# Optimization experiments

Measured on AMD Instinct MI355X. Metric: run time of the kernel, lower is better.

Reference implementation:

```python
import jax, jax.numpy as jnp
import numpy as np

DIM = 768; HEADS = 12; HD = DIM // HEADS; SCALE = HD ** -0.5
B = 4; T = 8; H = 14; W = 14; N = H * W  # 196 VMAE patches per frame
DOWN = 192   # adapter down dim = dim * 0.25
MLP_H = 3072 # dim * mlp_ratio

def _ln(x, g, b, eps=1e-5):
    m = x.mean(-1, keepdims=True)
    v = ((x - m) ** 2).mean(-1, keepdims=True)
    return (x - m) * jax.lax.rsqrt(v + eps) * g + b

def _lin(x, w, b=None):
    y = x @ w.T
    return y if b is None else y + b

def _gelu(x):
    return jax.nn.gelu(x, approximate=False)  # torch nn.GELU (erf)

def _mha(q, k, v):  # q:[b,h,n,d] k,v:[b,h,m,d]
    a = jax.nn.softmax((q * SCALE) @ jnp.swapaxes(k, -2, -1), axis=-1)
    return a @ v

def _adapter(x, w1, b1, w2, b2, skip):
    y = _lin(_gelu(_lin(x, w1, b1)), w2, b2)
    return x + y if skip else y

def _block(s_x, t_x, p):
    # --- self-attention on temporal (VMAE) tokens, with adapter ---
    xn = _ln(t_x, p['g1'], p['bb1'])
    bias = jnp.concatenate([p['q_bias'], jnp.zeros_like(p['v_bias']), p['v_bias']])
    Bx, Nx, _ = xn.shape
    qkv = _lin(xn, p['qkv_w'], bias).reshape(Bx, Nx, 3, HEADS, HD).transpose(2, 0, 3, 1, 4)
    o = _mha(qkv[0], qkv[1], qkv[2]).transpose(0, 2, 1, 3).reshape(Bx, Nx, DIM)
    o = _lin(o, p['aproj_w'], p['aproj_b'])
    t = t_x + _adapter(o, p['sa_w1'], p['sa_b1'], p['sa_w2'], p['sa_b2'], True)
    # --- S2T cross-attn: temporal queries attend to per-frame CNN spatial tokens ---
    s_pat = s_x.reshape(B * T, H * W, DIM) + p['s2t_pos_cnn']
    tx = t.reshape(B * T, N, DIM) + p['s2t_pos_vmae']
    q = _lin(tx, p['s2t_qw'], p['s2t_qb']).reshape(B * T, N, HEADS, HD).transpose(0, 2, 1, 3)
    kv = _lin(s_pat, p['s2t_kvw'], p['s2t_kvb']).reshape(B * T, H * W, 2, HEADS, HD).transpose(2, 0, 3, 1, 4)
    o = _mha(q, kv[0], kv[1]).transpose(0, 2, 1, 3).reshape(B * T, N, DIM)
    o = _lin(o, p['s2t_pw'], p['s2t_pb']).reshape(B, T * N, DIM)
    t = t + o
    # --- T2S cross-attn: per-location CNN queries attend over time to VMAE tokens ---
    s_pat = s_x.reshape(B, T, H * W, DIM).transpose(0, 2, 1, 3) + p['t2s_pos_cnn']  # b hw t c
    tx = t.reshape(B, T, N, DIM).transpose(0, 2, 1, 3) + p['t2s_pos_vmae']          # b n t d (N==H*W)
    s_pat = s_pat.reshape(B * H * W, T, DIM)
    tx = tx.reshape(B * N, T, DIM)
    q = _lin(s_pat, p['t2s_qw'], p['t2s_qb']).reshape(B * H * W, T, HEADS, HD).transpose(0, 2, 1, 3)
    kv = _lin(tx, p['t2s_kvw'], p['t2s_kvb']).reshape(B * N, T, 2, HEADS, HD).transpose(2, 0, 3, 1, 4)
    o = _mha(q, kv[0], kv[1]).transpose(0, 2, 1, 3).reshape(B * H * W, T, DIM)
    o = _lin(o, p['t2s_pw'], p['t2s_pb'])
    s = s_x + o.reshape(B, H, W, T, DIM).transpose(0, 3, 1, 2, 4).reshape(B * T, H, W, DIM)
    # --- MLP + parallel adapter (scale = 0.5 per Block.__init__) ---
    xn2 = _ln(t, p['g2'], p['bb2'])
    t = t + _lin(_gelu(_lin(xn2, p['fc1_w'], p['fc1_b'])), p['fc2_w'], p['fc2_b']) \
          + 0.5 * _adapter(xn2, p['ma_w1'], p['ma_b1'], p['ma_w2'], p['ma_b2'], False)
    return s, t

PARAM_NAMES = ['g1','bb1','qkv_w','q_bias','v_bias','aproj_w','aproj_b',
               'sa_w1','sa_b1','sa_w2','sa_b2',
               's2t_pos_cnn','s2t_pos_vmae','s2t_qw','s2t_qb','s2t_kvw','s2t_kvb','s2t_pw','s2t_pb',
               't2s_pos_cnn','t2s_pos_vmae','t2s_qw','t2s_qb','t2s_kvw','t2s_kvb','t2s_pw','t2s_pb',
               'g2','bb2','fc1_w','fc1_b','fc2_w','fc2_b','ma_w1','ma_b1','ma_w2','ma_b2']

def setup_inputs():
    key = jax.random.key(0)
    ks = iter(jax.random.split(key, 64))
    def w(shape, s=0.02):
        return jax.random.normal(next(ks), shape, jnp.float32) * s
    d = dict(
        s_x=jax.random.normal(next(ks), (B * T, H, W, DIM), jnp.float32),
        t_x=jax.random.normal(next(ks), (B, T * N, DIM), jnp.float32),
        g1=jnp.ones((DIM,), jnp.float32), bb1=jnp.zeros((DIM,), jnp.float32),
        qkv_w=w((3 * DIM, DIM)), q_bias=jnp.zeros((DIM,), jnp.float32), v_bias=jnp.zeros((DIM,), jnp.float32),
        aproj_w=w((DIM, DIM)), aproj_b=jnp.zeros((DIM,), jnp.float32),
        sa_w1=w((DOWN, DIM)), sa_b1=jnp.zeros((DOWN,), jnp.float32),
        sa_w2=w((DIM, DOWN)), sa_b2=jnp.zeros((DIM,), jnp.float32),
        s2t_pos_cnn=w((H * W, DIM), SCALE), s2t_pos_vmae=w((196, DIM), SCALE),
        s2t_qw=w((DIM, DIM)), s2t_qb=jnp.zeros((DIM,), jnp.float32),
        s2t_kvw=w((2 * DIM, DIM)), s2t_kvb=jnp.zeros((2 * DIM,), jnp.float32),
        s2t_pw=w((DIM, DIM)), s2t_pb=jnp.zeros((DIM,), jnp.float32),
        t2s_pos_cnn=w((T, DIM), SCALE), t2s_pos_vmae=w((T, DIM), SCALE),
        t2s_qw=w((DIM, DIM)), t2s_qb=jnp.zeros((DIM,), jnp.float32),
        t2s_kvw=w((2 * DIM, DIM)), t2s_kvb=jnp.zeros((2 * DIM,), jnp.float32),
        t2s_pw=w((DIM, DIM)), t2s_pb=jnp.zeros((DIM,), jnp.float32),
        g2=jnp.ones((DIM,), jnp.float32), bb2=jnp.zeros((DIM,), jnp.float32),
        fc1_w=w((MLP_H, DIM)), fc1_b=jnp.zeros((MLP_H,), jnp.float32),
        fc2_w=w((DIM, MLP_H)), fc2_b=jnp.zeros((DIM,), jnp.float32),
        ma_w1=w((DOWN, DIM)), ma_b1=jnp.zeros((DOWN,), jnp.float32),
        ma_w2=w((DIM, DOWN)), ma_b2=jnp.zeros((DIM,), jnp.float32),
    )
    return d

def reference(s_x, t_x, g1, bb1, qkv_w, q_bias, v_bias, aproj_w, aproj_b,
              sa_w1, sa_b1, sa_w2, sa_b2,
              s2t_pos_cnn, s2t_pos_vmae, s2t_qw, s2t_qb, s2t_kvw, s2t_kvb, s2t_pw, s2t_pb,
              t2s_pos_cnn, t2s_pos_vmae, t2s_qw, t2s_qb, t2s_kvw, t2s_kvb, t2s_pw, t2s_pb,
              g2, bb2, fc1_w, fc1_b, fc2_w, fc2_b, ma_w1, ma_b1, ma_w2, ma_b2):
    loc = locals()
    p = {k: loc[k] for k in PARAM_NAMES}
    return _block(s_x, t_x, p)
```

## Files before the change

### kernel.cpp

```cpp
#include <hip/hip_runtime.h>
#include <hip/hip_bf16.h>
#include <math.h>


typedef __bf16 bf16_t;
typedef bf16_t bf16x4 __attribute__((ext_vector_type(4)));
typedef bf16_t bf16x8 __attribute__((ext_vector_type(8)));
typedef float  f32x4  __attribute__((ext_vector_type(4)));

typedef const __attribute__((address_space(1))) void* gas_t;
typedef __attribute__((address_space(3))) void* las_t;
__device__ __forceinline__ void async16(const void* g, void* l) {
    __builtin_amdgcn_global_load_lds((gas_t)g, (las_t)l, 16, 0, 0);
}

#define MFMA(a,b,c) __builtin_amdgcn_mfma_f32_16x16x32_bf16((a),(b),(c),0,0,0)
#define EXP2(x) __builtin_amdgcn_exp2f(x)
#define LOG2E 1.4426950408889634f

template<bool GELU>
__global__ __launch_bounds__(256) void gemm128(
    const bf16_t* __restrict__ A, const bf16_t* __restrict__ W,
    const float* __restrict__ bias,
    const float* __restrict__ res1, const float* __restrict__ res2,
    float res2_scale,
    float* __restrict__ Yf, bf16_t* __restrict__ Yb,
    int M, int N, int K)
{
    __shared__ bf16_t As[128*64];
    __shared__ bf16_t Bs[128*64];
    const int tid = threadIdx.x, wave = tid >> 6, lane = tid & 63;
    const int m0 = blockIdx.y * 128, n0 = blockIdx.x * 128;
    const int wm = (wave & 1) * 64, wn = (wave >> 1) * 64;
    const int l15 = lane & 15, lq = lane >> 4;
    const int lrow = lane >> 3, lcol = (lane & 7) * 8;

    f32x4 acc[4][4] = {};

    for (int k0 = 0; k0 < K; k0 += 64) {
#pragma unroll
        for (int c = 0; c < 4; ++c) {
            const int r = wave * 32 + c * 8;
            async16(A + (size_t)(m0 + r + lrow) * K + k0 + lcol, &As[r * 64]);
            async16(W + (size_t)(n0 + r + lrow) * K + k0 + lcol, &Bs[r * 64]);
        }
        __syncthreads();
#pragma unroll
        for (int kk = 0; kk < 64; kk += 32) {
            bf16x8 a[4], b[4];
#pragma unroll
            for (int i = 0; i < 4; ++i)
                a[i] = *(const bf16x8*)&As[(wm + i * 16 + l15) * 64 + kk + lq * 8];
#pragma unroll
            for (int i = 0; i < 4; ++i)
                b[i] = *(const bf16x8*)&Bs[(wn + i * 16 + l15) * 64 + kk + lq * 8];
#pragma unroll
            for (int mi = 0; mi < 4; ++mi)
#pragma unroll
                for (int ni = 0; ni < 4; ++ni)
                    acc[mi][ni] = MFMA(a[mi], b[ni], acc[mi][ni]);
        }
        __syncthreads();
    }

#pragma unroll
    for (int mi = 0; mi < 4; ++mi)
#pragma unroll
    for (int ni = 0; ni < 4; ++ni) {
        const int gn = n0 + wn + ni * 16 + l15;
        const float bv = bias ? bias[gn] : 0.f;
#pragma unroll
        for (int i = 0; i < 4; ++i) {
            const int gm = m0 + wm + mi * 16 + lq * 4 + i;
            float v = acc[mi][ni][i] + bv;
            if (GELU) v = 0.5f * v * (1.0f + erff(v * 0.70710678118654752f));
            const size_t off = (size_t)gm * N + gn;
            if (res1) v += res1[off];
            if (res2) v += res2_scale * res2[off];
            if (Yf) Yf[off] = v;
            if (Yb) Yb[off] = (bf16_t)v;
        }
    }
}

template<bool GELU>
__global__ __launch_bounds__(256) void gemm128x64(
    const bf16_t* __restrict__ A, const bf16_t* __restrict__ W,
    const float* __restrict__ bias,
    const float* __restrict__ res1, const float* __restrict__ res2,
    float res2_scale,
    float* __restrict__ Yf, bf16_t* __restrict__ Yb,
    int M, int N, int K)
{
    __shared__ bf16_t As[128*64];
    __shared__ bf16_t Bs[64*64];
    const int tid = threadIdx.x, wave = tid >> 6, lane = tid & 63;
    const int m0 = blockIdx.y * 128, n0 = blockIdx.x * 64;
    const int wm = (wave & 1) * 64, wn = (wave >> 1) * 32;
    const int l15 = lane & 15, lq = lane >> 4;
    const int lrow = lane >> 3, lcol = (lane & 7) * 8;

    f32x4 acc[4][2] = {};

    for (int k0 = 0; k0 < K; k0 += 64) {
#pragma unroll
        for (int c = 0; c < 4; ++c) {
            const int r = wave * 32 + c * 8;
            async16(A + (size_t)(m0 + r + lrow) * K + k0 + lcol, &As[r * 64]);
        }
#pragma unroll
        for (int c = 0; c < 2; ++c) {
            const int r = wave * 16 + c * 8;
            async16(W + (size_t)(n0 + r + lrow) * K + k0 + lcol, &Bs[r * 64]);
        }
        __syncthreads();
#pragma unroll
        for (int kk = 0; kk < 64; kk += 32) {
            bf16x8 a[4], b[2];
#pragma unroll
            for (int i = 0; i < 4; ++i)
                a[i] = *(const bf16x8*)&As[(wm + i * 16 + l15) * 64 + kk + lq * 8];
#pragma unroll
            for (int i = 0; i < 2; ++i)
                b[i] = *(const bf16x8*)&Bs[(wn + i * 16 + l15) * 64 + kk + lq * 8];
#pragma unroll
            for (int mi = 0; mi < 4; ++mi)
#pragma unroll
                for (int ni = 0; ni < 2; ++ni)
                    acc[mi][ni] = MFMA(a[mi], b[ni], acc[mi][ni]);
        }
        __syncthreads();
    }

#pragma unroll
    for (int mi = 0; mi < 4; ++mi)
#pragma unroll
    for (int ni = 0; ni < 2; ++ni) {
        const int gn = n0 + wn + ni * 16 + l15;
        const float bv = bias ? bias[gn] : 0.f;
#pragma unroll
        for (int i = 0; i < 4; ++i) {
            const int gm = m0 + wm + mi * 16 + lq * 4 + i;
            float v = acc[mi][ni][i] + bv;
            if (GELU) v = 0.5f * v * (1.0f + erff(v * 0.70710678118654752f));
            const size_t off = (size_t)gm * N + gn;
            if (res1) v += res1[off];
            if (res2) v += res2_scale * res2[off];
            if (Yf) Yf[off] = v;
            if (Yb) Yb[off] = (bf16_t)v;
        }
    }
}

template<bool GELU>
__global__ __launch_bounds__(256) void gemm_bt(
    const float* __restrict__ X, const float* __restrict__ W,
    const float* __restrict__ bias,
    const float* __restrict__ res1, const float* __restrict__ res2,
    float res2_scale,
    float* __restrict__ Y, int M, int N, int K)
{
    __shared__ bf16_t As[64][72];
    __shared__ bf16_t Bs[64][72];
    const int tid  = threadIdx.x;
    const int n0   = blockIdx.x * 64;
    const int m0   = blockIdx.y * 64;
    const int wave = tid >> 6, lane = tid & 63;
    const int wm   = (wave & 1) * 32, wn = (wave >> 1) * 32;
    const int l15  = lane & 15, lq = lane >> 4;
    f32x4 acc[2][2] = {};
    const int sr = tid >> 4;
    const int sc4 = (tid & 15) * 4;

    for (int k0 = 0; k0 < K; k0 += 64) {
#pragma unroll
        for (int i = 0; i < 4; ++i) {
            const int row = sr + i * 16;
            const float4 xv = *reinterpret_cast<const float4*>(
                X + (size_t)(m0 + row) * K + k0 + sc4);
            bf16x4 p;
            p[0] = (bf16_t)xv.x; p[1] = (bf16_t)xv.y;
            p[2] = (bf16_t)xv.z; p[3] = (bf16_t)xv.w;
            *reinterpret_cast<bf16x4*>(&As[row][sc4]) = p;
        }
#pragma unroll
        for (int i = 0; i < 4; ++i) {
            const int row = sr + i * 16;
            const float4 wv = *reinterpret_cast<const float4*>(
                W + (size_t)(n0 + row) * K + k0 + sc4);
            bf16x4 p;
            p[0] = (bf16_t)wv.x; p[1] = (bf16_t)wv.y;
            p[2] = (bf16_t)wv.z; p[3] = (bf16_t)wv.w;
            *reinterpret_cast<bf16x4*>(&Bs[row][sc4]) = p;
        }
        __syncthreads();
#pragma unroll
        for (int kk = 0; kk < 64; kk += 32) {
            bf16x8 a0 = *reinterpret_cast<const bf16x8*>(&As[wm +      l15][kk + lq * 8]);
            bf16x8 a1 = *reinterpret_cast<const bf16x8*>(&As[wm + 16 + l15][kk + lq * 8]);
            bf16x8 b0 = *reinterpret_cast<const bf16x8*>(&Bs[wn +      l15][kk + lq * 8]);
            bf16x8 b1 = *reinterpret_cast<const bf16x8*>(&Bs[wn + 16 + l15][kk + lq * 8]);
            acc[0][0] = MFMA(a0, b0, acc[0][0]);
            acc[0][1] = MFMA(a0, b1, acc[0][1]);
            acc[1][0] = MFMA(a1, b0, acc[1][0]);
            acc[1][1] = MFMA(a1, b1, acc[1][1]);
        }
        __syncthreads();
    }

#pragma unroll
    for (int mt = 0; mt < 2; ++mt)
#pragma unroll
    for (int nt = 0; nt < 2; ++nt) {
        const int gn = n0 + wn + nt * 16 + l15;
        const float bv = bias[gn];
#pragma unroll
        for (int i = 0; i < 4; ++i) {
            const int gm = m0 + wm + mt * 16 + lq * 4 + i;
            float v = acc[mt][nt][i] + bv;
            if (GELU) v = 0.5f * v * (1.0f + erff(v * 0.70710678118654752f));
            const size_t off = (size_t)gm * N + gn;
            if (res1) v += res1[off];
            if (res2) v += res2_scale * res2[off];
            Y[off] = v;
        }
    }
}

__global__ __launch_bounds__(256) void flash_k(
    const bf16_t* __restrict__ Q, int ldq,
    const bf16_t* __restrict__ Kp, int ldk,
    const bf16_t* __restrict__ Vp, int ldv,
    bf16_t* __restrict__ O, int ldo,
    int nq, int nk, float scale)
{
    __shared__ bf16_t Qs[64 * 68];
    __shared__ bf16_t Ks[64 * 68];
    __shared__ bf16_t Vs[64 * 68];

    const int tid = threadIdx.x, wave = tid >> 6, lane = tid & 63;
    const int q0 = blockIdx.x * 64, hoff = blockIdx.y * 64, g = blockIdx.z;
    const int l15 = lane & 15, lq = lane >> 4;
    const int wm16 = wave * 16;
    const int sr = tid >> 3, sc8 = (tid & 7) * 8;
    const float sl2e = scale * LOG2E;

    {
        int r0 = q0 + sr;      if (r0 > nq - 1) r0 = nq - 1;
        int r1 = q0 + sr + 32; if (r1 > nq - 1) r1 = nq - 1;
        bf16x8 a = *(const bf16x8*)(Q + ((size_t)g * nq + r0) * ldq + hoff + sc8);
        bf16x8 b = *(const bf16x8*)(Q + ((size_t)g * nq + r1) * ldq + hoff + sc8);
        *(bf16x8*)&Qs[sr * 68 + sc8] = a;
        *(bf16x8*)&Qs[(sr + 32) * 68 + sc8] = b;
    }
    float mrow[4], lrow[4];
#pragma unroll
    for (int i = 0; i < 4; ++i) { mrow[i] = -INFINITY; lrow[i] = 0.f; }
    f32x4 acc[4] = {};

    for (int kk0 = 0; kk0 < nk; kk0 += 64) {
        __syncthreads();
        {
            int r0 = kk0 + sr;      if (r0 > nk - 1) r0 = nk - 1;
            int r1 = kk0 + sr + 32; if (r1 > nk - 1) r1 = nk - 1;
            bf16x8 a = *(const bf16x8*)(Kp + ((size_t)g * nk + r0) * ldk + hoff + sc8);
            bf16x8 b = *(const bf16x8*)(Kp + ((size_t)g * nk + r1) * ldk + hoff + sc8);
            *(bf16x8*)&Ks[sr * 68 + sc8] = a;
            *(bf16x8*)&Ks[(sr + 32) * 68 + sc8] = b;
            int key = kk0 + lane; if (key > nk - 1) key = nk - 1;
            const bf16_t* vp = Vp + ((size_t)g * nk + key) * ldv + hoff + wm16;
            bf16x8 v0 = *(const bf16x8*)vp;
            bf16x8 v1 = *(const bf16x8*)(vp + 8);
#pragma unroll
            for (int j = 0; j < 8; ++j) Vs[(wm16 + j) * 68 + lane] = v0[j];
#pragma unroll
            for (int j = 0; j < 8; ++j) Vs[(wm16 + 8 + j) * 68 + lane] = v1[j];
        }
        __syncthreads();

        f32x4 s[4] = {};
#pragma unroll
        for (int kk = 0; kk < 64; kk += 32) {
            bf16x8 a = *(const bf16x8*)&Qs[(wm16 + l15) * 68 + kk + lq * 8];
#pragma unroll
            for (int nt = 0; nt < 4; ++nt) {
                bf16x8 b = *(const bf16x8*)&Ks[(nt * 16 + l15) * 68 + kk + lq * 8];
                s[nt] = MFMA(a, b, s[nt]);
            }
        }
        __syncthreads();

#pragma unroll
        for (int nt = 0; nt < 4; ++nt) {
            const bool valid = (kk0 + nt * 16 + l15) < nk;
#pragma unroll
            for (int i = 0; i < 4; ++i)
                s[nt][i] = valid ? s[nt][i] * sl2e : -INFINITY;
        }
        float al[4];
#pragma unroll
        for (int i = 0; i < 4; ++i) {
            float t = fmaxf(fmaxf(s[0][i], s[1][i]), fmaxf(s[2][i], s[3][i]));
            t = fmaxf(t, __shfl_xor(t, 1));
            t = fmaxf(t, __shfl_xor(t, 2));
            t = fmaxf(t, __shfl_xor(t, 4));
            t = fmaxf(t, __shfl_xor(t, 8));
            const float mnew = fmaxf(mrow[i], t);
            const float a = EXP2(mrow[i] - mnew);
            float ps = 0.f;
#pragma unroll
            for (int nt = 0; nt < 4; ++nt) {
                const float e = EXP2(s[nt][i] - mnew);
                s[nt][i] = e; ps += e;
            }
            ps += __shfl_xor(ps, 1);
            ps += __shfl_xor(ps, 2);
            ps += __shfl_xor(ps, 4);
            ps += __shfl_xor(ps, 8);
            lrow[i] = lrow[i] * a + ps;
            mrow[i] = mnew; al[i] = a;
        }

#pragma unroll
        for (int nt = 0; nt < 4; ++nt)
#pragma unroll
        for (int i = 0; i < 4; ++i)
            Ks[(wm16 + lq * 4 + i) * 68 + nt * 16 + l15] = (bf16_t)s[nt][i];

#pragma unroll
        for (int nt = 0; nt < 4; ++nt)
#pragma unroll
        for (int i = 0; i < 4; ++i)
            acc[nt][i] *= al[i];
#pragma unroll
        for (int kk = 0; kk < 64; kk += 32) {
            bf16x8 a = *(const bf16x8*)&Ks[(wm16 + l15) * 68 + kk + lq * 8];
#pragma unroll
            for (int nt = 0; nt < 4; ++nt) {
                bf16x8 b = *(const bf16x8*)&Vs[(nt * 16 + l15) * 68 + kk + lq * 8];
                acc[nt] = MFMA(a, b, acc[nt]);
            }
        }
    }

#pragma unroll
    for (int nt = 0; nt < 4; ++nt)
#pragma unroll
    for (int i = 0; i < 4; ++i) {
        const int r = wm16 + lq * 4 + i, qrow = q0 + r;
        if (qrow < nq) {
            const float inv = __builtin_amdgcn_rcpf(lrow[i]);
            O[((size_t)g * nq + qrow) * ldo + hoff + nt * 16 + l15] =
                (bf16_t)(acc[nt][i] * inv);
        }
    }
}

__global__ __launch_bounds__(256) void attn8_k(
    const bf16_t* __restrict__ Q, int ldq,
    const bf16_t* __restrict__ Kp, int ldk,
    const bf16_t* __restrict__ Vp, int ldv,
    bf16_t* __restrict__ O, int ldo,
    float scale)
{
    __shared__ float Ps[4][8][8];
    const int wv = threadIdx.x >> 6, lane = threadIdx.x & 63;
    const int gw  = blockIdx.x * 4 + wv;
    const int seq = gw / 12, h = gw - seq * 12;
    const int hoff = h * 64;
    const int l15 = lane & 15, lq = lane >> 4;
    const size_t rbase = (size_t)seq * 8;
    const float sl2e = scale * LOG2E;

    const int qr = l15 & 7;
    const bf16_t* qp = Q  + (rbase + qr) * ldq + hoff + lq * 8;
    const bf16_t* kp = Kp + (rbase + qr) * ldk + hoff + lq * 8;
    bf16x8 a0 = *(const bf16x8*)qp;
    bf16x8 a1 = *(const bf16x8*)(qp + 32);
    bf16x8 b0 = *(const bf16x8*)kp;
    bf16x8 b1 = *(const bf16x8*)(kp + 32);
    f32x4 z = {};
    f32x4 s = MFMA(a1, b1, MFMA(a0, b0, z));

    const bool cvalid = l15 < 8;
    float p[4];
#pragma unroll
    for (int i = 0; i < 4; ++i) {
        float v = cvalid ? s[i] * sl2e : -INFINITY;
        float m = v;
        m = fmaxf(m, __shfl_xor(m, 1));
        m = fmaxf(m, __shfl_xor(m, 2));
        m = fmaxf(m, __shfl_xor(m, 4));
        m = fmaxf(m, __shfl_xor(m, 8));
        float e = EXP2(v - m);
        float sum = e;
        sum += __shfl_xor(sum, 1);
        sum += __shfl_xor(sum, 2);
        sum += __shfl_xor(sum, 4);
        sum += __shfl_xor(sum, 8);
        p[i] = e * __builtin_amdgcn_rcpf(sum);
    }
    if (lq < 2 && cvalid) {
#pragma unroll
        for (int i = 0; i < 4; ++i)
            Ps[wv][lq * 4 + i][l15] = p[i];
    }
    __syncthreads();

    const int qi = lane >> 3, dg = lane & 7;
    f32x4 p0 = *(const f32x4*)&Ps[wv][qi][0];
    f32x4 p1 = *(const f32x4*)&Ps[wv][qi][4];
    float acc[8] = {};
#pragma unroll
    for (int k = 0; k < 8; ++k) {
        const bf16x8 vvec = *(const bf16x8*)(Vp + (rbase + k) * ldv + hoff + dg * 8);
        const float pk = (k < 4) ? p0[k] : p1[k - 4];
#pragma unroll
        for (int j = 0; j < 8; ++j) acc[j] += pk * (float)vvec[j];
    }
    bf16x8 o;
#pragma unroll
    for (int j = 0; j < 8; ++j) o[j] = (bf16_t)acc[j];
    *(bf16x8*)(O + (rbase + qi) * ldo + hoff + dg * 8) = o;
}

__global__ __launch_bounds__(256) void ln_k(
    const float* __restrict__ x,
    const float* __restrict__ g, const float* __restrict__ bta,
    float* __restrict__ yf, bf16_t* __restrict__ yb)
{
    __shared__ float red[256], red2[256];
    __shared__ float s_m, s_r;
    const int row = blockIdx.x, tid = threadIdx.x;
    const size_t base = (size_t)row * 768;
    const float v0 = x[base + tid];
    const float v1 = x[base + tid + 256];
    const float v2 = x[base + tid + 512];
    red[tid]  = v0 + v1 + v2;
    red2[tid] = v0 * v0 + v1 * v1 + v2 * v2;
    __syncthreads();
    for (int st = 128; st > 0; st >>= 1) {
        if (tid < st) { red[tid] += red[tid + st]; red2[tid] += red2[tid + st]; }
        __syncthreads();
    }
    if (tid == 0) {
        const float m = red[0] * (1.f / 768.f);
        const float var = red2[0] * (1.f / 768.f) - m * m;
        s_m = m; s_r = rsqrtf(var + 1e-5f);
    }
    __syncthreads();
    const float m = s_m, r = s_r;
    const float o0 = (v0 - m) * r * g[tid]       + bta[tid];
    const float o1 = (v1 - m) * r * g[tid + 256] + bta[tid + 256];
    const float o2 = (v2 - m) * r * g[tid + 512] + bta[tid + 512];
    yb[base + tid]       = (bf16_t)o0;
    yb[base + tid + 256] = (bf16_t)o1;
    yb[base + tid + 512] = (bf16_t)o2;
    if (yf) {
        yf[base + tid]       = o0;
        yf[base + tid + 256] = o1;
        yf[base + tid + 512] = o2;
    }
}

__global__ void addpos_k(const float* __restrict__ src, const float* __restrict__ pos,
                         bf16_t* __restrict__ dst, int nrep) {
    const int row = blockIdx.x, tid = threadIdx.x;
    const size_t base = (size_t)row * 768;
    const size_t pbase = (size_t)(row % nrep) * 768;
    for (int k = 0; k < 3; ++k) {
        int c = tid + k * 256;
        dst[base + c] = (bf16_t)(src[base + c] + pos[pbase + c]);
    }
}
__global__ void t2s_prep_q(const float* __restrict__ sx, const float* __restrict__ pos,
                           bf16_t* __restrict__ dst) {
    const int row = blockIdx.x, tid = threadIdx.x;
    const int t = row & 7, bn = row >> 3, n = bn % 196, b = bn / 196;
    const size_t src = (size_t)((b * 8 + t) * 196 + n) * 768;
    const size_t dbase = (size_t)row * 768;
    const size_t pbase = (size_t)t * 768;
    for (int k = 0; k < 3; ++k) {
        int c = tid + k * 256;
        dst[dbase + c] = (bf16_t)(sx[src + c] + pos[pbase + c]);
    }
}
__global__ void t2s_prep_kv(const float* __restrict__ tcur, const float* __restrict__ pos,
                            bf16_t* __restrict__ dst) {
    const int row = blockIdx.x, tid = threadIdx.x;
    const int t = row & 7, bn = row >> 3, n = bn % 196, b = bn / 196;
    const size_t src = (size_t)(b * 1568 + t * 196 + n) * 768;
    const size_t dbase = (size_t)row * 768;
    const size_t pbase = (size_t)t * 768;
    for (int k = 0; k < 3; ++k) {
        int c = tid + k * 256;
        dst[dbase + c] = (bf16_t)(tcur[src + c] + pos[pbase + c]);
    }
}
__global__ void s_out_k(const float* __restrict__ sx, const float* __restrict__ o,
                        float* __restrict__ out) {
    const int row = blockIdx.x, tid = threadIdx.x;
    const int n = row % 196, bt = row / 196, t = bt & 7, b = bt >> 3;
    const size_t obase = (size_t)((b * 196 + n) * 8 + t) * 768;
    const size_t base = (size_t)row * 768;
    for (int k = 0; k < 3; ++k) {
        int c = tid + k * 256;
        out[base + c] = sx[base + c] + o[obase + c];
    }
}
__global__ void build_qkv_bias(const float* __restrict__ qb,
                               const float* __restrict__ vb,
                               float* __restrict__ dst) {
    int i = blockIdx.x * 256 + threadIdx.x;
    if (i < 768) dst[i] = qb[i];
    else if (i < 1536) dst[i] = 0.f;
    else if (i < 2304) dst[i] = vb[i - 1536];
}

struct WPtrs { const float* p[10]; };
__global__ void wcvt(WPtrs s, bf16_t* __restrict__ dst) {
    const int cum[11] = {0, 442368, 589824, 737280, 1032192, 1179648,
                         1327104, 1622016, 1769472, 2359296, 2949120};
    const int gi = blockIdx.x * 256 + threadIdx.x;
    int seg = 0;
#pragma unroll
    for (int i = 1; i < 10; ++i) if (gi >= cum[i]) seg = i;
    const float4 v = ((const float4*)s.p[seg])[gi - cum[seg]];
    bf16x4 o;
    o[0] = (bf16_t)v.x; o[1] = (bf16_t)v.y; o[2] = (bf16_t)v.z; o[3] = (bf16_t)v.w;
    ((bf16x4*)dst)[gi] = o;
}

#define OFF_QKV    0
#define OFF_APROJ  1769472
#define OFF_S2TQ   2359296
#define OFF_S2TKV  2949120
#define OFF_S2TP   4128768
#define OFF_T2SQ   4718592
#define OFF_T2SKV  5308416
#define OFF_T2SP   6488064
#define OFF_FC1    7077888
#define OFF_FC2    9437184
#define W_TOTAL    11796480

extern "C" void kernel_launch(void* const* d_in, const int* in_sizes, int n_in,
                              void* d_out, int out_size, void* d_ws, size_t ws_size,
                              hipStream_t stream)
{
    typedef const float* fp;
    fp s_x     = (fp)d_in[0];
    fp t_x     = (fp)d_in[1];
    fp g1      = (fp)d_in[2];
    fp bb1     = (fp)d_in[3];
    fp qkv_w   = (fp)d_in[4];
    fp q_bias  = (fp)d_in[5];
    fp v_bias  = (fp)d_in[6];
    fp aproj_w = (fp)d_in[7];
    fp aproj_b = (fp)d_in[8];
    fp sa_w1   = (fp)d_in[9];
    fp sa_b1   = (fp)d_in[10];
    fp sa_w2   = (fp)d_in[11];
    fp sa_b2   = (fp)d_in[12];
    fp s2t_pos_cnn  = (fp)d_in[13];
    fp s2t_pos_vmae = (fp)d_in[14];
    fp s2t_qw  = (fp)d_in[15];
    fp s2t_qb  = (fp)d_in[16];
    fp s2t_kvw = (fp)d_in[17];
    fp s2t_kvb = (fp)d_in[18];
    fp s2t_pw  = (fp)d_in[19];
    fp s2t_pb  = (fp)d_in[20];
    fp t2s_pos_cnn  = (fp)d_in[21];
    fp t2s_pos_vmae = (fp)d_in[22];
    fp t2s_qw  = (fp)d_in[23];
    fp t2s_qb  = (fp)d_in[24];
    fp t2s_kvw = (fp)d_in[25];
    fp t2s_kvb = (fp)d_in[26];
    fp t2s_pw  = (fp)d_in[27];
    fp t2s_pb  = (fp)d_in[28];
    fp g2      = (fp)d_in[29];
    fp bb2     = (fp)d_in[30];
    fp fc1_w   = (fp)d_in[31];
    fp fc1_b   = (fp)d_in[32];
    fp fc2_w   = (fp)d_in[33];
    fp fc2_b   = (fp)d_in[34];
    fp ma_w1   = (fp)d_in[35];
    fp ma_b1   = (fp)d_in[36];
    fp ma_w2   = (fp)d_in[37];
    fp ma_b2   = (fp)d_in[38];

    const size_t RD = (size_t)6272 * 768;

    float* ws   = (float*)d_ws;
    float* F    = ws;
    float* G    = F + RD;
    float* CI   = G + RD;
    float* Hb   = CI + RD;
    float* qkvb = Hb + (size_t)6272 * 192;
    bf16_t* BW  = (bf16_t*)(qkvb + 2304);
    bf16_t* Xb  = BW + W_TOTAL;
    bf16_t* Eb  = Xb + RD;
    bf16_t* Fb  = Eb + RD;
    bf16_t* MB  = Fb + RD;

    float* out_s = (float*)d_out;
    float* out_t = out_s + RD;

    const dim3 blk(256);

    WPtrs wp;
    wp.p[0] = qkv_w;  wp.p[1] = aproj_w; wp.p[2] = s2t_qw; wp.p[3] = s2t_kvw;
    wp.p[4] = s2t_pw; wp.p[5] = t2s_qw;  wp.p[6] = t2s_kvw; wp.p[7] = t2s_pw;
    wp.p[8] = fc1_w;  wp.p[9] = fc2_w;
    wcvt<<<11520, blk, 0, stream>>>(wp, BW);

    ln_k<<<6272, blk, 0, stream>>>(t_x, g1, bb1, nullptr, Xb);
    build_qkv_bias<<<9, blk, 0, stream>>>(q_bias, v_bias, qkvb);
    gemm128<false><<<dim3(18, 49), blk, 0, stream>>>(
        Xb, BW + OFF_QKV, qkvb, nullptr, nullptr, 0.f, nullptr, MB, 6272, 2304, 768);
    flash_k<<<dim3(25, 12, 4), blk, 0, stream>>>(
        MB, 2304, MB + 768, 2304, MB + 1536, 2304, Eb, 768, 1568, 1568, 0.125f);
    gemm128x64<false><<<dim3(12, 49), blk, 0, stream>>>(
        Eb, BW + OFF_APROJ, aproj_b, nullptr, nullptr, 0.f, F, nullptr, 6272, 768, 768);
    gemm_bt<true><<<dim3(3, 98), blk, 0, stream>>>(
        F, sa_w1, sa_b1, nullptr, nullptr, 0.f, Hb, 6272, 192, 768);
    gemm_bt<false><<<dim3(12, 98), blk, 0, stream>>>(
        Hb, sa_w2, sa_b2, F, t_x, 1.0f, G, 6272, 768, 192);

    addpos_k<<<6272, blk, 0, stream>>>(G, s2t_pos_vmae, Xb, 196);
    gemm128x64<false><<<dim3(12, 49), blk, 0, stream>>>(
        Xb, BW + OFF_S2TQ, s2t_qb, nullptr, nullptr, 0.f, nullptr, Eb, 6272, 768, 768);
    addpos_k<<<6272, blk, 0, stream>>>(s_x, s2t_pos_cnn, Xb, 196);
    gemm128<false><<<dim3(12, 49), blk, 0, stream>>>(
        Xb, BW + OFF_S2TKV, s2t_kvb, nullptr, nullptr, 0.f, nullptr, MB, 6272, 1536, 768);
    flash_k<<<dim3(4, 12, 32), blk, 0, stream>>>(
        Eb, 768, MB, 1536, MB + 768, 1536, Fb, 768, 196, 196, 0.125f);
    gemm128x64<false><<<dim3(12, 49), blk, 0, stream>>>(
        Fb, BW + OFF_S2TP, s2t_pb, G, nullptr, 0.f, G, nullptr, 6272, 768, 768);

    t2s_prep_q<<<6272, blk, 0, stream>>>(s_x, t2s_pos_cnn, Xb);
    gemm128x64<false><<<dim3(12, 49), blk, 0, stream>>>(
        Xb, BW + OFF_T2SQ, t2s_qb, nullptr, nullptr, 0.f, nullptr, Eb, 6272, 768, 768);
    t2s_prep_kv<<<6272, blk, 0, stream>>>(G, t2s_pos_vmae, Xb);
    gemm128<false><<<dim3(12, 49), blk, 0, stream>>>(
        Xb, BW + OFF_T2SKV, t2s_kvb, nullptr, nullptr, 0.f, nullptr, MB, 6272, 1536, 768);
    attn8_k<<<dim3(2352), blk, 0, stream>>>(
        Eb, 768, MB, 1536, MB + 768, 1536, Fb, 768, 0.125f);
    gemm128x64<false><<<dim3(12, 49), blk, 0, stream>>>(
        Fb, BW + OFF_T2SP, t2s_pb, nullptr, nullptr, 0.f, CI, nullptr, 6272, 768, 768);
    s_out_k<<<6272, blk, 0, stream>>>(s_x, CI, out_s);

    ln_k<<<6272, blk, 0, stream>>>(G, g2, bb2, CI, Xb);
    gemm128<true><<<dim3(24, 49), blk, 0, stream>>>(
        Xb, BW + OFF_FC1, fc1_b, nullptr, nullptr, 0.f, nullptr, MB, 6272, 3072, 768);
    gemm_bt<true><<<dim3(3, 98), blk, 0, stream>>>(
        CI, ma_w1, ma_b1, nullptr, nullptr, 0.f, Hb, 6272, 192, 768);
    gemm_bt<false><<<dim3(12, 98), blk, 0, stream>>>(
        Hb, ma_w2, ma_b2, nullptr, nullptr, 0.f, F, 6272, 768, 192);
    gemm128x64<false><<<dim3(12, 49), blk, 0, stream>>>(
        MB, BW + OFF_FC2, fc2_b, G, F, 0.5f, out_t, nullptr, 6272, 768, 3072);
}
```

Baseline: 991.7 us.

## Fuse pos-add and permute epilogues into GEMMs, prefetch K/V in flash attention

Three standalone elementwise kernels are folded into GEMM epilogues: the s2t position add, the t2s KV prep with its transpose, and the s_out residual with its permute. Each fused epilogue writes its extra bf16 or fp32 output directly with remapped row indices, saving full-size activation read/write passes and kernel launches at the cost of scattered stores. The flash attention kernel now register-prefetches the next K/V tile and uses a separate P buffer, which removes one barrier per iteration. The LayerNorm reduction is also changed to wavefront shuffles instead of a shared-memory tree.

```diff
diff --git a/kernel.cpp b/kernel.cpp
--- a/kernel.cpp
+++ b/kernel.cpp
@@ -83,14 +83,16 @@
     }
 }
 
-template<bool GELU>
+template<bool GELU, int EPI>
 __global__ __launch_bounds__(256) void gemm128x64(
     const bf16_t* __restrict__ A, const bf16_t* __restrict__ W,
     const float* __restrict__ bias,
     const float* __restrict__ res1, const float* __restrict__ res2,
     float res2_scale,
     float* __restrict__ Yf, bf16_t* __restrict__ Yb,
-    int M, int N, int K)
+    int M, int N, int K,
+    const float* __restrict__ ep_a, float* __restrict__ ep_fo,
+    bf16_t* __restrict__ ep_bo)
 {
     __shared__ bf16_t As[128*64];
     __shared__ bf16_t Bs[64*64];
@@ -148,17 +150,32 @@
             if (res2) v += res2_scale * res2[off];
             if (Yf) Yf[off] = v;
             if (Yb) Yb[off] = (bf16_t)v;
-        }
-    }
-}
-
-template<bool GELU>
+            if (EPI == 1) {
+                const int b_ = gm / 1568, r_ = gm - b_ * 1568;
+                const int t_ = r_ / 196,  n_ = r_ - t_ * 196;
+                const int dest = ((b_ * 196 + n_) << 3) + t_;
+                ep_bo[(size_t)dest * 768 + gn] =
+                    (bf16_t)(v + ep_a[t_ * 768 + gn]);
+            }
+            if (EPI == 2) {
+                const int t_ = gm & 7, bn_ = gm >> 3;
+                const int n_ = bn_ % 196, b_ = bn_ / 196;
+                const int dest = (b_ * 8 + t_) * 196 + n_;
+                const size_t doff = (size_t)dest * 768 + gn;
+                ep_fo[doff] = ep_a[doff] + v;
+            }
+        }
+    }
+}
+
+template<bool GELU, int EPI>
 __global__ __launch_bounds__(256) void gemm_bt(
     const float* __restrict__ X, const float* __restrict__ W,
     const float* __restrict__ bias,
     const float* __restrict__ res1, const float* __restrict__ res2,
     float res2_scale,
-    float* __restrict__ Y, int M, int N, int K)
+    float* __restrict__ Y, int M, int N, int K,
+    const float* __restrict__ ep_pos, bf16_t* __restrict__ ep_bo)
 {
     __shared__ bf16_t As[64][72];
     __shared__ bf16_t Bs[64][72];
@@ -223,6 +240,10 @@
             if (res1) v += res1[off];
             if (res2) v += res2_scale * res2[off];
             Y[off] = v;
+            if (EPI == 1) {
+                const int n_ = gm % 196;
+                ep_bo[off] = (bf16_t)(v + ep_pos[n_ * 768 + gn]);
+            }
         }
     }
 }
@@ -237,6 +258,7 @@
     __shared__ bf16_t Qs[64 * 68];
     __shared__ bf16_t Ks[64 * 68];
     __shared__ bf16_t Vs[64 * 68];
+    __shared__ bf16_t Ps[64 * 68];
 
     const int tid = threadIdx.x, wave = tid >> 6, lane = tid & 63;
     const int q0 = blockIdx.x * 64, hoff = blockIdx.y * 64, g = blockIdx.z;
@@ -253,6 +275,19 @@
         *(bf16x8*)&Qs[sr * 68 + sc8] = a;
         *(bf16x8*)&Qs[(sr + 32) * 68 + sc8] = b;
     }
+
+    bf16x8 ka, kb, va, vb;
+    {
+        int r0 = sr;      if (r0 > nk - 1) r0 = nk - 1;
+        int r1 = sr + 32; if (r1 > nk - 1) r1 = nk - 1;
+        ka = *(const bf16x8*)(Kp + ((size_t)g * nk + r0) * ldk + hoff + sc8);
+        kb = *(const bf16x8*)(Kp + ((size_t)g * nk + r1) * ldk + hoff + sc8);
+        int key = lane; if (key > nk - 1) key = nk - 1;
+        const bf16_t* vp = Vp + ((size_t)g * nk + key) * ldv + hoff + wm16;
+        va = *(const bf16x8*)vp;
+        vb = *(const bf16x8*)(vp + 8);
+    }
+
     float mrow[4], lrow[4];
 #pragma unroll
     for (int i = 0; i < 4; ++i) { mrow[i] = -INFINITY; lrow[i] = 0.f; }
@@ -260,23 +295,25 @@
 
     for (int kk0 = 0; kk0 < nk; kk0 += 64) {
         __syncthreads();
-        {
-            int r0 = kk0 + sr;      if (r0 > nk - 1) r0 = nk - 1;
-            int r1 = kk0 + sr + 32; if (r1 > nk - 1) r1 = nk - 1;
-            bf16x8 a = *(const bf16x8*)(Kp + ((size_t)g * nk + r0) * ldk + hoff + sc8);
-            bf16x8 b = *(const bf16x8*)(Kp + ((size_t)g * nk + r1) * ldk + hoff + sc8);
-            *(bf16x8*)&Ks[sr * 68 + sc8] = a;
-            *(bf16x8*)&Ks[(sr + 32) * 68 + sc8] = b;
-            int key = kk0 + lane; if (key > nk - 1) key = nk - 1;
+        *(bf16x8*)&Ks[sr * 68 + sc8] = ka;
+        *(bf16x8*)&Ks[(sr + 32) * 68 + sc8] = kb;
+#pragma unroll
+        for (int j = 0; j < 8; ++j) Vs[(wm16 + j) * 68 + lane] = va[j];
+#pragma unroll
+        for (int j = 0; j < 8; ++j) Vs[(wm16 + 8 + j) * 68 + lane] = vb[j];
+        __syncthreads();
+
+        const int nx = kk0 + 64;
+        if (nx < nk) {
+            int r0 = nx + sr;      if (r0 > nk - 1) r0 = nk - 1;
+            int r1 = nx + sr + 32; if (r1 > nk - 1) r1 = nk - 1;
+            ka = *(const bf16x8*)(Kp + ((size_t)g * nk + r0) * ldk + hoff + sc8);
+            kb = *(const bf16x8*)(Kp + ((size_t)g * nk + r1) * ldk + hoff + sc8);
+            int key = nx + lane; if (key > nk - 1) key = nk - 1;
             const bf16_t* vp = Vp + ((size_t)g * nk + key) * ldv + hoff + wm16;
-            bf16x8 v0 = *(const bf16x8*)vp;
-            bf16x8 v1 = *(const bf16x8*)(vp + 8);
-#pragma unroll
-            for (int j = 0; j < 8; ++j) Vs[(wm16 + j) * 68 + lane] = v0[j];
-#pragma unroll
-            for (int j = 0; j < 8; ++j) Vs[(wm16 + 8 + j) * 68 + lane] = v1[j];
-        }
-        __syncthreads();
+            va = *(const bf16x8*)vp;
+            vb = *(const bf16x8*)(vp + 8);
+        }
 
         f32x4 s[4] = {};
 #pragma unroll
@@ -288,7 +325,6 @@
                 s[nt] = MFMA(a, b, s[nt]);
             }
         }
-        __syncthreads();
 
 #pragma unroll
         for (int nt = 0; nt < 4; ++nt) {
@@ -325,7 +361,7 @@
         for (int nt = 0; nt < 4; ++nt)
 #pragma unroll
         for (int i = 0; i < 4; ++i)
-            Ks[(wm16 + lq * 4 + i) * 68 + nt * 16 + l15] = (bf16_t)s[nt][i];
+            Ps[(wm16 + lq * 4 + i) * 68 + nt * 16 + l15] = (bf16_t)s[nt][i];
 
 #pragma unroll
         for (int nt = 0; nt < 4; ++nt)
@@ -334,7 +370,7 @@
             acc[nt][i] *= al[i];
 #pragma unroll
         for (int kk = 0; kk < 64; kk += 32) {
-            bf16x8 a = *(const bf16x8*)&Ks[(wm16 + l15) * 68 + kk + lq * 8];
+            bf16x8 a = *(const bf16x8*)&Ps[(wm16 + l15) * 68 + kk + lq * 8];
 #pragma unroll
             for (int nt = 0; nt < 4; ++nt) {
                 bf16x8 b = *(const bf16x8*)&Vs[(nt * 16 + l15) * 68 + kk + lq * 8];
@@ -429,27 +465,26 @@
     const float* __restrict__ g, const float* __restrict__ bta,
     float* __restrict__ yf, bf16_t* __restrict__ yb)
 {
-    __shared__ float red[256], red2[256];
-    __shared__ float s_m, s_r;
+    __shared__ float rA[4], rB[4];
     const int row = blockIdx.x, tid = threadIdx.x;
+    const int wv = tid >> 6, lane = tid & 63;
     const size_t base = (size_t)row * 768;
     const float v0 = x[base + tid];
     const float v1 = x[base + tid + 256];
     const float v2 = x[base + tid + 512];
-    red[tid]  = v0 + v1 + v2;
-    red2[tid] = v0 * v0 + v1 * v1 + v2 * v2;
+    float s1 = v0 + v1 + v2;
+    float s2 = v0 * v0 + v1 * v1 + v2 * v2;
+#pragma unroll
+    for (int off = 32; off > 0; off >>= 1) {
+        s1 += __shfl_xor(s1, off);
+        s2 += __shfl_xor(s2, off);
+    }
+    if (lane == 0) { rA[wv] = s1; rB[wv] = s2; }
     __syncthreads();
-    for (int st = 128; st > 0; st >>= 1) {
-        if (tid < st) { red[tid] += red[tid + st]; red2[tid] += red2[tid + st]; }
-        __syncthreads();
-    }
-    if (tid == 0) {
-        const float m = red[0] * (1.f / 768.f);
-        const float var = red2[0] * (1.f / 768.f) - m * m;
-        s_m = m; s_r = rsqrtf(var + 1e-5f);
-    }
-    __syncthreads();
-    const float m = s_m, r = s_r;
+    const float ts1 = rA[0] + rA[1] + rA[2] + rA[3];
+    const float ts2 = rB[0] + rB[1] + rB[2] + rB[3];
+    const float m = ts1 * (1.f / 768.f);
+    const float r = rsqrtf(ts2 * (1.f / 768.f) - m * m + 1e-5f);
     const float o0 = (v0 - m) * r * g[tid]       + bta[tid];
     const float o1 = (v1 - m) * r * g[tid + 256] + bta[tid + 256];
     const float o2 = (v2 - m) * r * g[tid + 512] + bta[tid + 512];
@@ -483,29 +518,6 @@
     for (int k = 0; k < 3; ++k) {
         int c = tid + k * 256;
         dst[dbase + c] = (bf16_t)(sx[src + c] + pos[pbase + c]);
-    }
-}
-__global__ void t2s_prep_kv(const float* __restrict__ tcur, const float* __restrict__ pos,
-                            bf16_t* __restrict__ dst) {
-    const int row = blockIdx.x, tid = threadIdx.x;
-    const int t = row & 7, bn = row >> 3, n = bn % 196, b = bn / 196;
-    const size_t src = (size_t)(b * 1568 + t * 196 + n) * 768;
-    const size_t dbase = (size_t)row * 768;
-    const size_t pbase = (size_t)t * 768;
-    for (int k = 0; k < 3; ++k) {
-        int c = tid + k * 256;
-        dst[dbase + c] = (bf16_t)(tcur[src + c] + pos[pbase + c]);
-    }
-}
-__global__ void s_out_k(const float* __restrict__ sx, const float* __restrict__ o,
-                        float* __restrict__ out) {
-    const int row = blockIdx.x, tid = threadIdx.x;
-    const int n = row % 196, bt = row / 196, t = bt & 7, b = bt >> 3;
-    const size_t obase = (size_t)((b * 196 + n) * 8 + t) * 768;
-    const size_t base = (size_t)row * 768;
-    for (int k = 0; k < 3; ++k) {
-        int c = tid + k * 256;
-        out[base + c] = sx[base + c] + o[obase + c];
     }
 }
 __global__ void build_qkv_bias(const float* __restrict__ qb,
@@ -601,6 +613,7 @@
     bf16_t* Eb  = Xb + RD;
     bf16_t* Fb  = Eb + RD;
     bf16_t* MB  = Fb + RD;
+    bf16_t* Xkv = MB + (size_t)6272 * 1536;
 
     float* out_s = (float*)d_out;
     float* out_t = out_s + RD;
@@ -619,43 +632,46 @@
         Xb, BW + OFF_QKV, qkvb, nullptr, nullptr, 0.f, nullptr, MB, 6272, 2304, 768);
     flash_k<<<dim3(25, 12, 4), blk, 0, stream>>>(
         MB, 2304, MB + 768, 2304, MB + 1536, 2304, Eb, 768, 1568, 1568, 0.125f);
-    gemm128x64<false><<<dim3(12, 49), blk, 0, stream>>>(
-        Eb, BW + OFF_APROJ, aproj_b, nullptr, nullptr, 0.f, F, nullptr, 6272, 768, 768);
-    gemm_bt<true><<<dim3(3, 98), blk, 0, stream>>>(
-        F, sa_w1, sa_b1, nullptr, nullptr, 0.f, Hb, 6272, 192, 768);
-    gemm_bt<false><<<dim3(12, 98), blk, 0, stream>>>(
-        Hb, sa_w2, sa_b2, F, t_x, 1.0f, G, 6272, 768, 192);
-
-    addpos_k<<<6272, blk, 0, stream>>>(G, s2t_pos_vmae, Xb, 196);
-    gemm128x64<false><<<dim3(12, 49), blk, 0, stream>>>(
-        Xb, BW + OFF_S2TQ, s2t_qb, nullptr, nullptr, 0.f, nullptr, Eb, 6272, 768, 768);
+    gemm128x64<false, 0><<<dim3(12, 49), blk, 0, stream>>>(
+        Eb, BW + OFF_APROJ, aproj_b, nullptr, nullptr, 0.f, F, nullptr, 6272, 768, 768,
+        nullptr, nullptr, nullptr);
+    gemm_bt<true, 0><<<dim3(3, 98), blk, 0, stream>>>(
+        F, sa_w1, sa_b1, nullptr, nullptr, 0.f, Hb, 6272, 192, 768, nullptr, nullptr);
+    gemm_bt<false, 1><<<dim3(12, 98), blk, 0, stream>>>(
+        Hb, sa_w2, sa_b2, F, t_x, 1.0f, G, 6272, 768, 192, s2t_pos_vmae, Xb);
+
+    gemm128x64<false, 0><<<dim3(12, 49), blk, 0, stream>>>(
+        Xb, BW + OFF_S2TQ, s2t_qb, nullptr, nullptr, 0.f, nullptr, Eb, 6272, 768, 768,
+        nullptr, nullptr, nullptr);
     addpos_k<<<6272, blk, 0, stream>>>(s_x, s2t_pos_cnn, Xb, 196);
     gemm128<false><<<dim3(12, 49), blk, 0, stream>>>(
         Xb, BW + OFF_S2TKV, s2t_kvb, nullptr, nullptr, 0.f, nullptr, MB, 6272, 1536, 768);
     flash_k<<<dim3(4, 12, 32), blk, 0, stream>>>(
         Eb, 768, MB, 1536, MB + 768, 1536, Fb, 768, 196, 196, 0.125f);
-    gemm128x64<false><<<dim3(12, 49), blk, 0, stream>>>(
-        Fb, BW + OFF_S2TP, s2t_pb, G, nullptr, 0.f, G, nullptr, 6272, 768, 768);
+    gemm128x64<false, 1><<<dim3(12, 49), blk, 0, stream>>>(
+        Fb, BW + OFF_S2TP, s2t_pb, G, nullptr, 0.f, G, nullptr, 6272, 768, 768,
+        t2s_pos_vmae, nullptr, Xkv);
 
     t2s_prep_q<<<6272, blk, 0, stream>>>(s_x, t2s_pos_cnn, Xb);
-    gemm128x64<false><<<dim3(12, 49), blk, 0, stream>>>(
-        Xb, BW + OFF_T2SQ, t2s_qb, nullptr, nullptr, 0.f, nullptr, Eb, 6272, 768, 768);
-    t2s_prep_kv<<<6272, blk, 0, stream>>>(G, t2s_pos_vmae, Xb);
+    gemm128x64<false, 0><<<dim3(12, 49), blk, 0, stream>>>(
+        Xb, BW + OFF_T2SQ, t2s_qb, nullptr, nullptr, 0.f, nullptr, Eb, 6272, 768, 768,
+        nullptr, nullptr, nullptr);
     gemm128<false><<<dim3(12, 49), blk, 0, stream>>>(
-        Xb, BW + OFF_T2SKV, t2s_kvb, nullptr, nullptr, 0.f, nullptr, MB, 6272, 1536, 768);
+        Xkv, BW + OFF_T2SKV, t2s_kvb, nullptr, nullptr, 0.f, nullptr, MB, 6272, 1536, 768);
     attn8_k<<<dim3(2352), blk, 0, stream>>>(
         Eb, 768, MB, 1536, MB + 768, 1536, Fb, 768, 0.125f);
-    gemm128x64<false><<<dim3(12, 49), blk, 0, stream>>>(
-        Fb, BW + OFF_T2SP, t2s_pb, nullptr, nullptr, 0.f, CI, nullptr, 6272, 768, 768);
-    s_out_k<<<6272, blk, 0, stream>>>(s_x, CI, out_s);
+    gemm128x64<false, 2><<<dim3(12, 49), blk, 0, stream>>>(
+        Fb, BW + OFF_T2SP, t2s_pb, nullptr, nullptr, 0.f, nullptr, nullptr, 6272, 768, 768,
+        s_x, out_s, nullptr);
 
     ln_k<<<6272, blk, 0, stream>>>(G, g2, bb2, CI, Xb);
     gemm128<true><<<dim3(24, 49), blk, 0, stream>>>(
         Xb, BW + OFF_FC1, fc1_b, nullptr, nullptr, 0.f, nullptr, MB, 6272, 3072, 768);
-    gemm_bt<true><<<dim3(3, 98), blk, 0, stream>>>(
-        CI, ma_w1, ma_b1, nullptr, nullptr, 0.f, Hb, 6272, 192, 768);
-    gemm_bt<false><<<dim3(12, 98), blk, 0, stream>>>(
-        Hb, ma_w2, ma_b2, nullptr, nullptr, 0.f, F, 6272, 768, 192);
-    gemm128x64<false><<<dim3(12, 49), blk, 0, stream>>>(
-        MB, BW + OFF_FC2, fc2_b, G, F, 0.5f, out_t, nullptr, 6272, 768, 3072);
-}
+    gemm_bt<true, 0><<<dim3(3, 98), blk, 0, stream>>>(
+        CI, ma_w1, ma_b1, nullptr, nullptr, 0.f, Hb, 6272, 192, 768, nullptr, nullptr);
+    gemm_bt<false, 0><<<dim3(12, 98), blk, 0, stream>>>(
+        Hb, ma_w2, ma_b2, nullptr, nullptr, 0.f, F, 6272, 768, 192, nullptr, nullptr);
+    gemm128x64<false, 0><<<dim3(12, 49), blk, 0, stream>>>(
+        MB, BW + OFF_FC2, fc2_b, G, F, 0.5f, out_t, nullptr, 6272, 768, 3072,
+        nullptr, nullptr, nullptr);
+}
```

Result: no change. 979.0 us (-1.3%).
